# Kernel tuning notes

Hardware: AMD Instinct MI355X
Metric: run time of the kernel (lower is better)

## Reference

```python
import jax, jax.numpy as jnp
import numpy as np

HEADS = 8
LN_EPS = 1e-5


def _layernorm(x, g, b):
    mu = x.mean(-1, keepdims=True)
    var = jnp.var(x, axis=-1, keepdims=True)  # biased, matches torch LayerNorm
    return (x - mu) / jnp.sqrt(var + LN_EPS) * g + b


def setup_inputs() -> dict:
    key = jax.random.key(0)
    ks = jax.random.split(key, 5)
    Q, N, D = 4, 2048, 512  # [query-groups, tokens, model dim]
    return {
        "q": jax.random.normal(ks[0], (Q, N, D), jnp.float32),
        "k": jax.random.normal(ks[1], (Q, N, D), jnp.float32),
        "v": jax.random.normal(ks[2], (Q, N, D), jnp.float32),
        "ln_gamma": jnp.ones((D,), jnp.float32),
        "ln_beta": jnp.zeros((D,), jnp.float32),
        "w_in": jax.random.normal(ks[3], (D, D), jnp.float32) * 0.02,   # torch Linear weight [inner_dim, dim]
        "w_out": jax.random.normal(ks[4], (D, D), jnp.float32) * 0.02,  # [dim, inner_dim]
        "b_out": jnp.zeros((D,), jnp.float32),
        "cov_w_raw": jnp.float32(0.6),
        "var_w_raw": jnp.float32(0.2),
    }


def reference(q, k, v, ln_gamma, ln_beta, w_in, w_out, b_out, cov_w_raw, var_w_raw):
    H = HEADS

    def proj(t):
        x = _layernorm(t, ln_gamma, ln_beta) @ w_in.T  # [Q,N,inner]
        Qd, Nd, I = x.shape
        return x.reshape(Qd, Nd, H, I // H).transpose(2, 0, 1, 3)  # [H,Q,N,d]

    f_q, f_k, f_v = proj(q), proj(k), proj(v)
    d = f_q.shape[-1]

    # cosine similarity component
    dots = jnp.einsum('hqnd,hqmd->hqnm', f_q, f_k)
    qn = jnp.linalg.norm(f_q, axis=-1)  # [H,Q,N]
    kn = jnp.linalg.norm(f_k, axis=-1)
    cosine_sim = dots / (qn[..., :, None] * kn[..., None, :])

    # centered covariance component
    qc = f_q - f_q.mean(-1, keepdims=True)
    kc = f_k - f_k.mean(-1, keepdims=True)
    cov_component = jnp.einsum('hqnd,hqmd->hqnm', qc, kc) / d

    # variance product component (torch.var is unbiased -> ddof=1)
    q_var = jnp.var(f_q, axis=-1, ddof=1)  # [H,Q,N]
    k_var = jnp.var(f_k, axis=-1, ddof=1)
    var_component = q_var[..., :, None] * k_var[..., None, :] / d

    cov_w = jax.nn.sigmoid(cov_w_raw)
    var_w = jax.nn.sigmoid(var_w_raw)
    cos_w = 1.0 - cov_w - var_w
    attn = cos_w * cosine_sim + cov_w * cov_component + var_w * var_component

    out = jnp.einsum('hqnm,hqmd->hqnd', attn, f_v)
    out = out.transpose(1, 2, 0, 3).reshape(q.shape[0], q.shape[1], -1)  # q n (h d)
    return out @ w_out.T + b_out
```

## Files before the change

kernel.cpp:

```cpp
#include <hip/hip_runtime.h>
#include <hip/hip_bf16.h>
#include <math.h>

#define D_MODEL 512
#define NTOK 2048
#define QGRP 4
#define NHEAD 8
#define HDIM 64
#define ROWS_PER_T (QGRP * NTOK)
#define LN_EPS 1e-5f
#define NCHUNK 16

typedef __attribute__((ext_vector_type(8))) short short8;
typedef __attribute__((ext_vector_type(8))) __bf16 bf16x8;
typedef __attribute__((ext_vector_type(4))) float f32x4;

__device__ inline void split2(float y, ushort& h, ushort& l) {
    __hip_bfloat16 hb = __float2bfloat16(y);
    float hf = __bfloat162float(hb);
    __hip_bfloat16 lb = __float2bfloat16(y - hf);
    h = *reinterpret_cast<ushort*>(&hb);
    l = *reinterpret_cast<ushort*>(&lb);
}

__device__ inline float b2f(ushort u) {
    unsigned int x = ((unsigned int)u) << 16;
    return __uint_as_float(x);
}

__device__ inline void split8v(const float4& p0, const float4& p1, bf16x8& bh, bf16x8& bl) {
    float xv[8] = {p0.x, p0.y, p0.z, p0.w, p1.x, p1.y, p1.z, p1.w};
    ushort hs[8], ls[8];
#pragma unroll
    for (int j = 0; j < 8; ++j) split2(xv[j], hs[j], ls[j]);
    bh = *(const bf16x8*)hs;
    bl = *(const bf16x8*)ls;
}

__global__ __launch_bounds__(256)
void ln_split3_kernel(const float* __restrict__ q, const float* __restrict__ k,
                      const float* __restrict__ v, const float* __restrict__ gamma,
                      const float* __restrict__ beta,
                      ushort* __restrict__ A3h, ushort* __restrict__ A3l) {
    int wave = threadIdx.x >> 6, lane = threadIdx.x & 63;
    size_t row = (size_t)blockIdx.x * 4 + wave;
    int t = (int)(row >> 13);
    size_t r = row & 8191;
    const float* src = (t == 0 ? q : (t == 1 ? k : v)) + r * D_MODEL + lane * 8;
    float4 a = *(const float4*)src;
    float4 b = *(const float4*)(src + 4);
    float s  = a.x + a.y + a.z + a.w + b.x + b.y + b.z + b.w;
    float sq = a.x*a.x + a.y*a.y + a.z*a.z + a.w*a.w
             + b.x*b.x + b.y*b.y + b.z*b.z + b.w*b.w;
    for (int m = 1; m < 64; m <<= 1) {
        s  += __shfl_xor(s, m);
        sq += __shfl_xor(sq, m);
    }
    float mu   = s * (1.0f / (float)D_MODEL);
    float var  = sq * (1.0f / (float)D_MODEL) - mu * mu;
    float rstd = 1.0f / sqrtf(var + LN_EPS);
    float4 g0 = *(const float4*)(gamma + lane * 8);
    float4 g1 = *(const float4*)(gamma + lane * 8 + 4);
    float4 t0 = *(const float4*)(beta + lane * 8);
    float4 t1 = *(const float4*)(beta + lane * 8 + 4);
    float xv[8] = {a.x, a.y, a.z, a.w, b.x, b.y, b.z, b.w};
    float gv[8] = {g0.x, g0.y, g0.z, g0.w, g1.x, g1.y, g1.z, g1.w};
    float bv[8] = {t0.x, t0.y, t0.z, t0.w, t1.x, t1.y, t1.z, t1.w};
    ushort hs[8], ls[8];
#pragma unroll
    for (int j = 0; j < 8; ++j) {
        float y = (xv[j] - mu) * rstd * gv[j] + bv[j];
        split2(y, hs[j], ls[j]);
    }
    *(short8*)(A3h + row * D_MODEL + lane * 8) = *(const short8*)hs;
    *(short8*)(A3l + row * D_MODEL + lane * 8) = *(const short8*)ls;
}

__global__ __launch_bounds__(256)
void split_mat2_kernel(const float* __restrict__ W0, const float* __restrict__ W1,
                       ushort* __restrict__ Wh0, ushort* __restrict__ Wl0,
                       ushort* __restrict__ Wh1, ushort* __restrict__ Wl1) {
    int half = blockIdx.x >> 7;
    const float* W = half ? W1 : W0;
    ushort* Wh = half ? Wh1 : Wh0;
    ushort* Wl = half ? Wl1 : Wl0;
    size_t i = ((size_t)(blockIdx.x & 127) * 256 + threadIdx.x) * 8;
    float4 a = *(const float4*)(W + i);
    float4 b = *(const float4*)(W + i + 4);
    float xv[8] = {a.x, a.y, a.z, a.w, b.x, b.y, b.z, b.w};
    ushort hs[8], ls[8];
#pragma unroll
    for (int j = 0; j < 8; ++j) split2(xv[j], hs[j], ls[j]);
    *(short8*)(Wh + i) = *(const short8*)hs;
    *(short8*)(Wl + i) = *(const short8*)ls;
}

template <int MODE>
__global__ __launch_bounds__(256, 2)
void gemm_split_kernel(const ushort* __restrict__ Ah, const ushort* __restrict__ Al,
                       const ushort* __restrict__ Wh, const ushort* __restrict__ Wl,
                       const float* __restrict__ bias, float* __restrict__ C,
                       ushort* __restrict__ Ch, ushort* __restrict__ Cl) {
    __shared__ __align__(16) ushort sA[2][128][64];
    __shared__ __align__(16) ushort sW[2][128][64];
    int tid  = threadIdx.x;
    int lane = tid & 63, wid = tid >> 6;
    int wr = wid >> 1, wc = wid & 1;
    int z, xblk;
    if (MODE == 3) { z = blockIdx.x % 3; xblk = blockIdx.x / 3; }
    else           { z = 0;              xblk = blockIdx.x;     }
    size_t rowBase = (size_t)xblk * 128;
    size_t colBase = (size_t)blockIdx.y * 128;
    size_t zoff = (size_t)z * ROWS_PER_T * D_MODEL;
    const ushort* gA[2] = {Ah + zoff, Al + zoff};
    const ushort* gW[2] = {Wh, Wl};

    int sr = tid >> 3;
    int sc8 = tid & 7;

    short8 st[16];

#define LOADK(KT)                                                                  \
    {                                                                              \
        int idx = 0;                                                               \
        _Pragma("unroll")                                                          \
        for (int hl = 0; hl < 2; ++hl)                                             \
            _Pragma("unroll")                                                      \
            for (int p = 0; p < 4; ++p) {                                          \
                int r = p * 32 + sr;                                               \
                st[idx++] = *(const short8*)(gA[hl] + (rowBase + r) * D_MODEL +    \
                                             (KT) + sc8 * 8);                      \
            }                                                                      \
        _Pragma("unroll")                                                          \
        for (int hl = 0; hl < 2; ++hl)                                             \
            _Pragma("unroll")                                                      \
            for (int p = 0; p < 4; ++p) {                                          \
                int r = p * 32 + sr;                                               \
                st[idx++] = *(const short8*)(gW[hl] + (colBase + r) * D_MODEL +    \
                                             (KT) + sc8 * 8);                      \
            }                                                                      \
    }

    f32x4 acc[4][4] = {};

    LOADK(0);
    for (int step = 0; step < 8; ++step) {
        __syncthreads();
        {
            int idx = 0;
#pragma unroll
            for (int hl = 0; hl < 2; ++hl)
#pragma unroll
                for (int p = 0; p < 4; ++p) {
                    int r = p * 32 + sr;
                    *(short8*)&sA[hl][r][((sc8 ^ (r & 7)) << 3)] = st[idx++];
                }
#pragma unroll
            for (int hl = 0; hl < 2; ++hl)
#pragma unroll
                for (int p = 0; p < 4; ++p) {
                    int r = p * 32 + sr;
                    *(short8*)&sW[hl][r][((sc8 ^ (r & 7)) << 3)] = st[idx++];
                }
        }
        __syncthreads();
        if (step < 7) LOADK((step + 1) * 64);
#pragma unroll
        for (int sl = 0; sl < 2; ++sl) {
            bf16x8 aH[4], aL[4];
#pragma unroll
            for (int m = 0; m < 4; ++m) {
                int r = wr * 64 + m * 16 + (lane & 15);
                int cs = ((sl * 4 + (lane >> 4)) ^ (r & 7)) << 3;
                aH[m] = *(const bf16x8*)&sA[0][r][cs];
                aL[m] = *(const bf16x8*)&sA[1][r][cs];
            }
#pragma unroll
            for (int n = 0; n < 4; ++n) {
                int r = wc * 64 + n * 16 + (lane & 15);
                int cs = ((sl * 4 + (lane >> 4)) ^ (r & 7)) << 3;
                bf16x8 bH = *(const bf16x8*)&sW[0][r][cs];
                bf16x8 bL = *(const bf16x8*)&sW[1][r][cs];
#pragma unroll
                for (int m = 0; m < 4; ++m) {
                    acc[m][n] = __builtin_amdgcn_mfma_f32_16x16x32_bf16(aL[m], bH, acc[m][n], 0, 0, 0);
                    acc[m][n] = __builtin_amdgcn_mfma_f32_16x16x32_bf16(aH[m], bL, acc[m][n], 0, 0, 0);
                    acc[m][n] = __builtin_amdgcn_mfma_f32_16x16x32_bf16(aH[m], bH, acc[m][n], 0, 0, 0);
                }
            }
        }
    }
#pragma unroll
    for (int m = 0; m < 4; ++m)
#pragma unroll
        for (int n = 0; n < 4; ++n) {
            size_t col = colBase + wc * 64 + n * 16 + (lane & 15);
            size_t rb  = rowBase + wr * 64 + m * 16 + ((lane >> 4) << 2);
            if (MODE == 3) {
                if (z == 0) {
#pragma unroll
                    for (int r = 0; r < 4; ++r) {
                        ushort oh, ol;
                        split2(acc[m][n][r], oh, ol);
                        Ch[(rb + r) * D_MODEL + col] = oh;
                        Cl[(rb + r) * D_MODEL + col] = ol;
                    }
                } else {
                    float* Cz = C + (size_t)(z - 1) * ROWS_PER_T * D_MODEL;
#pragma unroll
                    for (int r = 0; r < 4; ++r)
                        Cz[(rb + r) * D_MODEL + col] = acc[m][n][r];
                }
            } else {
                float bv = bias[col];
#pragma unroll
                for (int r = 0; r < 4; ++r)
                    C[(rb + r) * D_MODEL + col] = acc[m][n][r] + bv;
            }
        }
#undef LOADK
}

__global__ __launch_bounds__(256)
void pair_reduce_mfma_kernel(const float* __restrict__ fk, const float* __restrict__ fv,
                             float* __restrict__ partials) {
    int pc = blockIdx.x;
    int pair = pc >> 4, chunk = pc & 15;
    int h = pair & 7, qg = pair >> 3;
    const float* Fk = fk + ((size_t)(qg * NTOK + chunk * 128)) * D_MODEL + h * HDIM;
    const float* Fv = fv + ((size_t)(qg * NTOK + chunk * 128)) * D_MODEL + h * HDIM;
    __shared__ float fkT[64][132];
    __shared__ float fvT[64][132];
    __shared__ float rkn_s[128], kvar_s[128];
    __shared__ float uvp[4][64];
    int tid = threadIdx.x, lane = tid & 63, wid = tid >> 6;
    int tn = tid >> 2;
    int fb = (tid & 3) << 2;
#pragma unroll
    for (int pass = 0; pass < 2; ++pass) {
        int n = pass * 64 + tn;
        float x[16], y[16];
#pragma unroll
        for (int j4 = 0; j4 < 4; ++j4) {
            *(float4*)&x[j4 * 4] = *(const float4*)(Fk + (size_t)n * D_MODEL + fb + j4 * 16);
            *(float4*)&y[j4 * 4] = *(const float4*)(Fv + (size_t)n * D_MODEL + fb + j4 * 16);
        }
        float s = 0.f, sq = 0.f;
#pragma unroll
        for (int j = 0; j < 16; ++j) { s += x[j]; sq += x[j] * x[j]; }
        s  += __shfl_xor(s, 1);  s  += __shfl_xor(s, 2);
        sq += __shfl_xor(sq, 1); sq += __shfl_xor(sq, 2);
        if ((tid & 3) == 0) {
            rkn_s[n]  = 1.0f / sqrtf(sq);
            kvar_s[n] = (sq - s * s * (1.0f / 64.0f)) * (1.0f / 63.0f);
        }
#pragma unroll
        for (int j4 = 0; j4 < 4; ++j4)
#pragma unroll
            for (int i = 0; i < 4; ++i) {
                fkT[fb + j4 * 16 + i][n] = x[j4 * 4 + i];
                fvT[fb + j4 * 16 + i][n] = y[j4 * 4 + i];
            }
    }
    __syncthreads();

    {
        float acc = 0.f;
#pragma unroll
        for (int j4 = 0; j4 < 8; ++j4) {
            float4 kv  = *(const float4*)&kvar_s[wid * 32 + j4 * 4];
            float4 f4  = *(const float4*)&fvT[lane][wid * 32 + j4 * 4];
            acc += kv.x * f4.x + kv.y * f4.y + kv.z * f4.z + kv.w * f4.w;
        }
        uvp[wid][lane] = acc;
    }

    int wm = wid >> 1, wn = wid & 1;
    int fr = lane & 15, kg = (lane >> 4) << 3;
    f32x4 accP[2][2] = {}, accC[2][2] = {};
#pragma unroll
    for (int t = 0; t < 4; ++t) {
        int k0 = t * 32 + kg;
        float4 rk0 = *(const float4*)&rkn_s[k0];
        float4 rk1 = *(const float4*)&rkn_s[k0 + 4];
        bf16x8 aRH[2], aRL[2], aSH[2], aSL[2], bH[2], bL[2];
#pragma unroll
        for (int m = 0; m < 2; ++m) {
            int a = wm * 32 + m * 16 + fr;
            float4 r0 = *(const float4*)&fkT[a][k0];
            float4 r1 = *(const float4*)&fkT[a][k0 + 4];
            split8v(r0, r1, aRH[m], aRL[m]);
            float4 s0 = make_float4(r0.x * rk0.x, r0.y * rk0.y, r0.z * rk0.z, r0.w * rk0.w);
            float4 s1 = make_float4(r1.x * rk1.x, r1.y * rk1.y, r1.z * rk1.z, r1.w * rk1.w);
            split8v(s0, s1, aSH[m], aSL[m]);
        }
#pragma unroll
        for (int n = 0; n < 2; ++n) {
            int c = wn * 32 + n * 16 + fr;
            float4 r0 = *(const float4*)&fvT[c][k0];
            float4 r1 = *(const float4*)&fvT[c][k0 + 4];
            split8v(r0, r1, bH[n], bL[n]);
        }
#pragma unroll
        for (int m = 0; m < 2; ++m)
#pragma unroll
            for (int n = 0; n < 2; ++n) {
                accP[m][n] = __builtin_amdgcn_mfma_f32_16x16x32_bf16(aSL[m], bH[n], accP[m][n], 0, 0, 0);
                accP[m][n] = __builtin_amdgcn_mfma_f32_16x16x32_bf16(aSH[m], bL[n], accP[m][n], 0, 0, 0);
                accP[m][n] = __builtin_amdgcn_mfma_f32_16x16x32_bf16(aSH[m], bH[n], accP[m][n], 0, 0, 0);
                accC[m][n] = __builtin_amdgcn_mfma_f32_16x16x32_bf16(aRL[m], bH[n], accC[m][n], 0, 0, 0);
                accC[m][n] = __builtin_amdgcn_mfma_f32_16x16x32_bf16(aRH[m], bL[n], accC[m][n], 0, 0, 0);
                accC[m][n] = __builtin_amdgcn_mfma_f32_16x16x32_bf16(aRH[m], bH[n], accC[m][n], 0, 0, 0);
            }
    }

    float* outp = partials + (size_t)pc * 8256;
#pragma unroll
    for (int m = 0; m < 2; ++m)
#pragma unroll
        for (int n = 0; n < 2; ++n) {
            int a0 = wm * 32 + m * 16 + ((lane >> 4) << 2);
            int c  = wn * 32 + n * 16 + fr;
#pragma unroll
            for (int r = 0; r < 4; ++r) {
                outp[(a0 + r) * 64 + c]        = accP[m][n][r];
                outp[4096 + (a0 + r) * 64 + c] = accC[m][n][r];
            }
        }
    __syncthreads();
    if (tid < 64)
        outp[8192 + tid] = uvp[0][tid] + uvp[1][tid] + uvp[2][tid] + uvp[3][tid];
}

__global__ __launch_bounds__(256)
void pair_finalize_kernel(const float* __restrict__ partials, float* __restrict__ pairacc) {
    int pair = blockIdx.x >> 3, sl = blockIdx.x & 7;
    int e0 = sl * 1032, e1 = e0 + 1032;
    for (int e = e0 + threadIdx.x; e < e1; e += 256) {
        float s = 0.f;
        for (int c = 0; c < NCHUNK; ++c)
            s += partials[((size_t)(pair * NCHUNK + c)) * 8256 + e];
        pairacc[(size_t)pair * 8320 + e] = s;
    }
}

__global__ __launch_bounds__(256)
void q_apply_mfma_kernel(const ushort* __restrict__ Fqh, const ushort* __restrict__ Fql,
                         const float* __restrict__ pairacc,
                         const float* __restrict__ cov_raw, const float* __restrict__ var_raw,
                         ushort* __restrict__ Oh, ushort* __restrict__ Ol) {
    int pair = blockIdx.x >> 4, chunk = blockIdx.x & 15;
    int h = pair & 7, qg = pair >> 3;
    __shared__ float PT[64][68];
    __shared__ float CT[64][68];
    __shared__ float u_s[64], sc_s[64];
    const float* pa = pairacc + (size_t)pair * 8320;
    for (int e = threadIdx.x; e < 4096; e += 256) {
        int a = e >> 6, c = e & 63;
        PT[c][a] = pa[e];
        CT[c][a] = pa[4096 + e];
    }
    if (threadIdx.x < 64) u_s[threadIdx.x] = pa[8192 + threadIdx.x];
    __syncthreads();
    if (threadIdx.x < 64) {
        float s = 0.f;
#pragma unroll
        for (int a = 0; a < 64; ++a) s += CT[threadIdx.x][a];
        sc_s[threadIdx.x] = s;
    }
    __syncthreads();
    int tid = threadIdx.x, lane = tid & 63, wave = tid >> 6;
    size_t row0 = (size_t)qg * NTOK + (size_t)chunk * 128 + wave * 32;
    const ushort* qhp = Fqh + row0 * D_MODEL + h * HDIM;
    const ushort* qlp = Fql + row0 * D_MODEL + h * HDIM;

    bf16x8 aH[2][2], aL[2][2];
    float qsum[2], qsq[2];
#pragma unroll
    for (int m = 0; m < 2; ++m) {
        int r = m * 16 + (lane & 15);
        int k0 = (lane >> 4) * 8;
        float s = 0.f, sq = 0.f;
#pragma unroll
        for (int ks = 0; ks < 2; ++ks) {
            short8 hv = *(const short8*)(qhp + (size_t)r * D_MODEL + ks * 32 + k0);
            short8 lv = *(const short8*)(qlp + (size_t)r * D_MODEL + ks * 32 + k0);
            aH[m][ks] = *(const bf16x8*)&hv;
            aL[m][ks] = *(const bf16x8*)&lv;
#pragma unroll
            for (int j = 0; j < 8; ++j) {
                float val = b2f((ushort)hv[j]) + b2f((ushort)lv[j]);
                s += val; sq += val * val;
            }
        }
        s  += __shfl_xor(s, 16);  s  += __shfl_xor(s, 32);
        sq += __shfl_xor(sq, 16); sq += __shfl_xor(sq, 32);
        qsum[m] = s; qsq[m] = sq;
    }

    f32x4 accP[2][4] = {}, accC[2][4] = {};
#pragma unroll
    for (int n = 0; n < 4; ++n) {
        int c = n * 16 + (lane & 15);
#pragma unroll
        for (int ks = 0; ks < 2; ++ks) {
            int kb = ks * 32 + (lane >> 4) * 8;
            {
                float4 p0 = *(const float4*)&PT[c][kb];
                float4 p1 = *(const float4*)&PT[c][kb + 4];
                bf16x8 bH, bL;
                split8v(p0, p1, bH, bL);
#pragma unroll
                for (int m = 0; m < 2; ++m) {
                    accP[m][n] = __builtin_amdgcn_mfma_f32_16x16x32_bf16(aL[m][ks], bH, accP[m][n], 0, 0, 0);
                    accP[m][n] = __builtin_amdgcn_mfma_f32_16x16x32_bf16(aH[m][ks], bL, accP[m][n], 0, 0, 0);
                    accP[m][n] = __builtin_amdgcn_mfma_f32_16x16x32_bf16(aH[m][ks], bH, accP[m][n], 0, 0, 0);
                }
            }
            {
                float4 p0 = *(const float4*)&CT[c][kb];
                float4 p1 = *(const float4*)&CT[c][kb + 4];
                bf16x8 bH, bL;
                split8v(p0, p1, bH, bL);
#pragma unroll
                for (int m = 0; m < 2; ++m) {
                    accC[m][n] = __builtin_amdgcn_mfma_f32_16x16x32_bf16(aL[m][ks], bH, accC[m][n], 0, 0, 0);
                    accC[m][n] = __builtin_amdgcn_mfma_f32_16x16x32_bf16(aH[m][ks], bL, accC[m][n], 0, 0, 0);
                    accC[m][n] = __builtin_amdgcn_mfma_f32_16x16x32_bf16(aH[m][ks], bH, accC[m][n], 0, 0, 0);
                }
            }
        }
    }

    float cw = 1.0f / (1.0f + expf(-cov_raw[0]));
    float vw = 1.0f / (1.0f + expf(-var_raw[0]));
    float cos_w = 1.0f - cw - vw;
    float cw_cov = cw * (1.0f / 64.0f);
    float cw_var = vw * (1.0f / 64.0f);
#pragma unroll
    for (int n = 0; n < 4; ++n) {
        int c = n * 16 + (lane & 15);
        float u_c  = u_s[c];
        float sc_c = sc_s[c];
#pragma unroll
        for (int m = 0; m < 2; ++m)
#pragma unroll
            for (int i = 0; i < 4; ++i) {
                int rp = ((lane >> 4) << 2) + i;
                float s  = __shfl(qsum[m], rp);
                float sq = __shfl(qsq[m], rp);
                float qmean = s * (1.0f / 64.0f);
                float rqn   = 1.0f / sqrtf(sq);
                float qvar  = (sq - s * qmean) * (1.0f / 63.0f);
                float res = cos_w * rqn * accP[m][n][i]
                          + cw_cov * (accC[m][n][i] - qmean * sc_c)
                          + cw_var * qvar * u_c;
                ushort oh, ol;
                split2(res, oh, ol);
                size_t o = (row0 + m * 16 + rp) * D_MODEL + h * HDIM + c;
                Oh[o] = oh;
                Ol[o] = ol;
            }
    }
}

extern "C" void kernel_launch(void* const* d_in, const int* in_sizes, int n_in,
                              void* d_out, int out_size, void* d_ws, size_t ws_size,
                              hipStream_t stream) {
    const float* q     = (const float*)d_in[0];
    const float* k     = (const float*)d_in[1];
    const float* v     = (const float*)d_in[2];
    const float* gamma = (const float*)d_in[3];
    const float* beta  = (const float*)d_in[4];
    const float* w_in  = (const float*)d_in[5];
    const float* w_out = (const float*)d_in[6];
    const float* b_out = (const float*)d_in[7];
    const float* cov_r = (const float*)d_in[8];
    const float* var_r = (const float*)d_in[9];
    float* out = (float*)d_out;

    const size_t E = (size_t)ROWS_PER_T * D_MODEL;
    float*  ws       = (float*)d_ws;
    float*  fk       = ws;
    float*  fv       = fk + E;
    ushort* Fqh      = (ushort*)(fv + E);
    ushort* Fql      = Fqh + E;
    ushort* A3h      = Fql + E;
    ushort* A3l      = A3h + 3 * E;
    ushort* Whi      = A3l + 3 * E;
    ushort* Wli      = Whi + D_MODEL * D_MODEL;
    ushort* Who      = Wli + D_MODEL * D_MODEL;
    ushort* Wlo      = Who + D_MODEL * D_MODEL;
    ushort* Oh       = Wlo + D_MODEL * D_MODEL;
    ushort* Ol       = Oh + E;
    float*  partials = (float*)(Ol + E);
    float*  pairacc  = partials + (size_t)32 * NCHUNK * 8256;

    hipLaunchKernelGGL(split_mat2_kernel, dim3(256), dim3(256), 0, stream,
                       w_in, w_out, Whi, Wli, Who, Wlo);
    hipLaunchKernelGGL(ln_split3_kernel, dim3(3 * ROWS_PER_T / 4), dim3(256), 0, stream,
                       q, k, v, gamma, beta, A3h, A3l);
    hipLaunchKernelGGL((gemm_split_kernel<3>), dim3(192, 4), dim3(256), 0, stream,
                       A3h, A3l, Whi, Wli, (const float*)nullptr, fk, Fqh, Fql);
    hipLaunchKernelGGL(pair_reduce_mfma_kernel, dim3(32 * NCHUNK), dim3(256), 0, stream,
                       fk, fv, partials);
    hipLaunchKernelGGL(pair_finalize_kernel, dim3(32 * 8), dim3(256), 0, stream,
                       partials, pairacc);
    hipLaunchKernelGGL(q_apply_mfma_kernel, dim3(512), dim3(256), 0, stream,
                       Fqh, Fql, pairacc, cov_r, var_r, Oh, Ol);
    hipLaunchKernelGGL((gemm_split_kernel<2>), dim3(ROWS_PER_T / 128, 4), dim3(256), 0, stream,
                       Oh, Ol, Who, Wlo, b_out, out, (ushort*)nullptr, (ushort*)nullptr);
}
```

Measured before the change: 117.0 us.

## Fuse LayerNorm and bf16 split into input projection GEMM prologue

The separate LayerNorm+split kernel is removed. The projection GEMM now reads fp32 q/k/v directly, computes per-row mean and rstd in a prologue, and normalizes and splits into hi/lo bf16 while staging tiles into shared memory. This drops the write and re-read of the 3x bf16 hi/lo activation buffers. The GEMM also moves to 512 threads with 8 waves of 64x32 tiles instead of 4 waves of 64x64, which lowers per-thread register pressure. In exchange, each block re-reads its rows for the statistics pass, the normalization is recomputed once per column block (4x), and the old occupancy hint of 2 blocks per CU is dropped.

```diff
diff --git a/kernel.cpp b/kernel.cpp
--- a/kernel.cpp
+++ b/kernel.cpp
@@ -35,45 +35,6 @@
     for (int j = 0; j < 8; ++j) split2(xv[j], hs[j], ls[j]);
     bh = *(const bf16x8*)hs;
     bl = *(const bf16x8*)ls;
-}
-
-__global__ __launch_bounds__(256)
-void ln_split3_kernel(const float* __restrict__ q, const float* __restrict__ k,
-                      const float* __restrict__ v, const float* __restrict__ gamma,
-                      const float* __restrict__ beta,
-                      ushort* __restrict__ A3h, ushort* __restrict__ A3l) {
-    int wave = threadIdx.x >> 6, lane = threadIdx.x & 63;
-    size_t row = (size_t)blockIdx.x * 4 + wave;
-    int t = (int)(row >> 13);
-    size_t r = row & 8191;
-    const float* src = (t == 0 ? q : (t == 1 ? k : v)) + r * D_MODEL + lane * 8;
-    float4 a = *(const float4*)src;
-    float4 b = *(const float4*)(src + 4);
-    float s  = a.x + a.y + a.z + a.w + b.x + b.y + b.z + b.w;
-    float sq = a.x*a.x + a.y*a.y + a.z*a.z + a.w*a.w
-             + b.x*b.x + b.y*b.y + b.z*b.z + b.w*b.w;
-    for (int m = 1; m < 64; m <<= 1) {
-        s  += __shfl_xor(s, m);
-        sq += __shfl_xor(sq, m);
-    }
-    float mu   = s * (1.0f / (float)D_MODEL);
-    float var  = sq * (1.0f / (float)D_MODEL) - mu * mu;
-    float rstd = 1.0f / sqrtf(var + LN_EPS);
-    float4 g0 = *(const float4*)(gamma + lane * 8);
-    float4 g1 = *(const float4*)(gamma + lane * 8 + 4);
-    float4 t0 = *(const float4*)(beta + lane * 8);
-    float4 t1 = *(const float4*)(beta + lane * 8 + 4);
-    float xv[8] = {a.x, a.y, a.z, a.w, b.x, b.y, b.z, b.w};
-    float gv[8] = {g0.x, g0.y, g0.z, g0.w, g1.x, g1.y, g1.z, g1.w};
-    float bv[8] = {t0.x, t0.y, t0.z, t0.w, t1.x, t1.y, t1.z, t1.w};
-    ushort hs[8], ls[8];
-#pragma unroll
-    for (int j = 0; j < 8; ++j) {
-        float y = (xv[j] - mu) * rstd * gv[j] + bv[j];
-        split2(y, hs[j], ls[j]);
-    }
-    *(short8*)(A3h + row * D_MODEL + lane * 8) = *(const short8*)hs;
-    *(short8*)(A3l + row * D_MODEL + lane * 8) = *(const short8*)ls;
 }
 
 __global__ __launch_bounds__(256)
@@ -96,75 +57,138 @@
 }
 
 template <int MODE>
-__global__ __launch_bounds__(256, 2)
-void gemm_split_kernel(const ushort* __restrict__ Ah, const ushort* __restrict__ Al,
+__global__ __launch_bounds__(512)
+void gemm_split_kernel(const float* __restrict__ Qp, const float* __restrict__ Kp,
+                       const float* __restrict__ Vp,
+                       const float* __restrict__ gamma, const float* __restrict__ beta,
+                       const ushort* __restrict__ Ahx, const ushort* __restrict__ Alx,
                        const ushort* __restrict__ Wh, const ushort* __restrict__ Wl,
                        const float* __restrict__ bias, float* __restrict__ C,
                        ushort* __restrict__ Ch, ushort* __restrict__ Cl) {
     __shared__ __align__(16) ushort sA[2][128][64];
     __shared__ __align__(16) ushort sW[2][128][64];
+    __shared__ float sG[512], sB[512];
+    __shared__ float mu_s[128], rs_s[128];
+
     int tid  = threadIdx.x;
     int lane = tid & 63, wid = tid >> 6;
-    int wr = wid >> 1, wc = wid & 1;
+    int wr = wid >> 2, wc = wid & 3;
     int z, xblk;
     if (MODE == 3) { z = blockIdx.x % 3; xblk = blockIdx.x / 3; }
     else           { z = 0;              xblk = blockIdx.x;     }
     size_t rowBase = (size_t)xblk * 128;
     size_t colBase = (size_t)blockIdx.y * 128;
-    size_t zoff = (size_t)z * ROWS_PER_T * D_MODEL;
-    const ushort* gA[2] = {Ah + zoff, Al + zoff};
+
+    const float* srcA = nullptr;
+    const ushort* gAh = nullptr; const ushort* gAl = nullptr;
+    if (MODE == 3) {
+        srcA = (z == 0 ? Qp : (z == 1 ? Kp : Vp)) + rowBase * D_MODEL;
+    } else {
+        gAh = Ahx + rowBase * D_MODEL;
+        gAl = Alx + rowBase * D_MODEL;
+    }
     const ushort* gW[2] = {Wh, Wl};
 
-    int sr = tid >> 3;
-    int sc8 = tid & 7;
-
-    short8 st[16];
-
-#define LOADK(KT)                                                                  \
-    {                                                                              \
-        int idx = 0;                                                               \
-        _Pragma("unroll")                                                          \
-        for (int hl = 0; hl < 2; ++hl)                                             \
-            _Pragma("unroll")                                                      \
-            for (int p = 0; p < 4; ++p) {                                          \
-                int r = p * 32 + sr;                                               \
-                st[idx++] = *(const short8*)(gA[hl] + (rowBase + r) * D_MODEL +    \
-                                             (KT) + sc8 * 8);                      \
-            }                                                                      \
-        _Pragma("unroll")                                                          \
-        for (int hl = 0; hl < 2; ++hl)                                             \
-            _Pragma("unroll")                                                      \
-            for (int p = 0; p < 4; ++p) {                                          \
-                int r = p * 32 + sr;                                               \
-                st[idx++] = *(const short8*)(gW[hl] + (colBase + r) * D_MODEL +    \
-                                             (KT) + sc8 * 8);                      \
-            }                                                                      \
-    }
-
-    f32x4 acc[4][4] = {};
+    int sr = tid >> 3, sc8 = tid & 7;
+
+    float4 stA[2][2];
+    short8 stA16[2][2];
+    short8 stW[2][2];
+
+#define LOADK(KT)                                                                    \
+    {                                                                                \
+        if (MODE == 3) {                                                             \
+            _Pragma("unroll")                                                        \
+            for (int p = 0; p < 2; ++p) {                                            \
+                int r = p * 64 + sr;                                                 \
+                const float* ap = srcA + (size_t)r * D_MODEL + (KT) + sc8 * 8;       \
+                stA[p][0] = *(const float4*)ap;                                      \
+                stA[p][1] = *(const float4*)(ap + 4);                                \
+            }                                                                        \
+        } else {                                                                     \
+            _Pragma("unroll")                                                        \
+            for (int hl = 0; hl < 2; ++hl)                                           \
+                _Pragma("unroll")                                                    \
+                for (int p = 0; p < 2; ++p) {                                        \
+                    int r = p * 64 + sr;                                             \
+                    stA16[hl][p] = *(const short8*)((hl ? gAl : gAh) +               \
+                                    (size_t)r * D_MODEL + (KT) + sc8 * 8);           \
+                }                                                                    \
+        }                                                                            \
+        _Pragma("unroll")                                                            \
+        for (int hl = 0; hl < 2; ++hl)                                               \
+            _Pragma("unroll")                                                        \
+            for (int p = 0; p < 2; ++p) {                                            \
+                int r = p * 64 + sr;                                                 \
+                stW[hl][p] = *(const short8*)(gW[hl] + (colBase + r) * D_MODEL +     \
+                                              (KT) + sc8 * 8);                       \
+            }                                                                        \
+    }
 
     LOADK(0);
+
+    if (MODE == 3) {
+        sG[tid] = gamma[tid];
+        sB[tid] = beta[tid];
+        int r = tid >> 2, qd = tid & 3;
+        const float* rp = srcA + (size_t)r * D_MODEL + qd * 128;
+        float s = 0.f, sq = 0.f;
+#pragma unroll
+        for (int j = 0; j < 32; ++j) {
+            float4 a4 = *(const float4*)(rp + j * 4);
+            s  += a4.x + a4.y + a4.z + a4.w;
+            sq += a4.x*a4.x + a4.y*a4.y + a4.z*a4.z + a4.w*a4.w;
+        }
+        s  += __shfl_xor(s, 1);  s  += __shfl_xor(s, 2);
+        sq += __shfl_xor(sq, 1); sq += __shfl_xor(sq, 2);
+        if (qd == 0) {
+            float mu = s * (1.0f / (float)D_MODEL);
+            mu_s[r] = mu;
+            rs_s[r] = rsqrtf(sq * (1.0f / (float)D_MODEL) - mu * mu + LN_EPS);
+        }
+    }
+
+    f32x4 acc[4][2] = {};
+
     for (int step = 0; step < 8; ++step) {
+        int KT = step * 64;
         __syncthreads();
-        {
-            int idx = 0;
+        if (MODE == 3) {
+#pragma unroll
+            for (int p = 0; p < 2; ++p) {
+                int r = p * 64 + sr;
+                float mu = mu_s[r], rs = rs_s[r];
+                float xv[8];
+                *(float4*)&xv[0] = stA[p][0];
+                *(float4*)&xv[4] = stA[p][1];
+                ushort hs[8], ls[8];
+#pragma unroll
+                for (int j = 0; j < 8; ++j) {
+                    int cc = KT + sc8 * 8 + j;
+                    float yv = (xv[j] - mu) * rs * sG[cc] + sB[cc];
+                    split2(yv, hs[j], ls[j]);
+                }
+                *(short8*)&sA[0][r][(sc8 ^ (r & 7)) << 3] = *(const short8*)hs;
+                *(short8*)&sA[1][r][(sc8 ^ (r & 7)) << 3] = *(const short8*)ls;
+            }
+        } else {
 #pragma unroll
             for (int hl = 0; hl < 2; ++hl)
 #pragma unroll
-                for (int p = 0; p < 4; ++p) {
-                    int r = p * 32 + sr;
-                    *(short8*)&sA[hl][r][((sc8 ^ (r & 7)) << 3)] = st[idx++];
+                for (int p = 0; p < 2; ++p) {
+                    int r = p * 64 + sr;
+                    *(short8*)&sA[hl][r][(sc8 ^ (r & 7)) << 3] = stA16[hl][p];
                 }
-#pragma unroll
-            for (int hl = 0; hl < 2; ++hl)
-#pragma unroll
-                for (int p = 0; p < 4; ++p) {
-                    int r = p * 32 + sr;
-                    *(short8*)&sW[hl][r][((sc8 ^ (r & 7)) << 3)] = st[idx++];
-                }
-        }
+        }
+#pragma unroll
+        for (int hl = 0; hl < 2; ++hl)
+#pragma unroll
+            for (int p = 0; p < 2; ++p) {
+                int r = p * 64 + sr;
+                *(short8*)&sW[hl][r][(sc8 ^ (r & 7)) << 3] = stW[hl][p];
+            }
         __syncthreads();
-        if (step < 7) LOADK((step + 1) * 64);
+        if (step < 7) LOADK(KT + 64);
 #pragma unroll
         for (int sl = 0; sl < 2; ++sl) {
             bf16x8 aH[4], aL[4];
@@ -176,11 +200,11 @@
                 aL[m] = *(const bf16x8*)&sA[1][r][cs];
             }
 #pragma unroll
-            for (int n = 0; n < 4; ++n) {
-                int r = wc * 64 + n * 16 + (lane & 15);
-                int cs = ((sl * 4 + (lane >> 4)) ^ (r & 7)) << 3;
-                bf16x8 bH = *(const bf16x8*)&sW[0][r][cs];
-                bf16x8 bL = *(const bf16x8*)&sW[1][r][cs];
+            for (int n = 0; n < 2; ++n) {
+                int rc = wc * 32 + n * 16 + (lane & 15);
+                int cs = ((sl * 4 + (lane >> 4)) ^ (rc & 7)) << 3;
+                bf16x8 bH = *(const bf16x8*)&sW[0][rc][cs];
+                bf16x8 bL = *(const bf16x8*)&sW[1][rc][cs];
 #pragma unroll
                 for (int m = 0; m < 4; ++m) {
                     acc[m][n] = __builtin_amdgcn_mfma_f32_16x16x32_bf16(aL[m], bH, acc[m][n], 0, 0, 0);
@@ -193,8 +217,8 @@
 #pragma unroll
     for (int m = 0; m < 4; ++m)
 #pragma unroll
-        for (int n = 0; n < 4; ++n) {
-            size_t col = colBase + wc * 64 + n * 16 + (lane & 15);
+        for (int n = 0; n < 2; ++n) {
+            size_t col = colBase + wc * 32 + n * 16 + (lane & 15);
             size_t rb  = rowBase + wr * 64 + m * 16 + ((lane >> 4) << 2);
             if (MODE == 3) {
                 if (z == 0) {
@@ -485,9 +509,7 @@
     float*  fv       = fk + E;
     ushort* Fqh      = (ushort*)(fv + E);
     ushort* Fql      = Fqh + E;
-    ushort* A3h      = Fql + E;
-    ushort* A3l      = A3h + 3 * E;
-    ushort* Whi      = A3l + 3 * E;
+    ushort* Whi      = Fql + E;
     ushort* Wli      = Whi + D_MODEL * D_MODEL;
     ushort* Who      = Wli + D_MODEL * D_MODEL;
     ushort* Wlo      = Who + D_MODEL * D_MODEL;
@@ -498,16 +520,17 @@
 
     hipLaunchKernelGGL(split_mat2_kernel, dim3(256), dim3(256), 0, stream,
                        w_in, w_out, Whi, Wli, Who, Wlo);
-    hipLaunchKernelGGL(ln_split3_kernel, dim3(3 * ROWS_PER_T / 4), dim3(256), 0, stream,
-                       q, k, v, gamma, beta, A3h, A3l);
-    hipLaunchKernelGGL((gemm_split_kernel<3>), dim3(192, 4), dim3(256), 0, stream,
-                       A3h, A3l, Whi, Wli, (const float*)nullptr, fk, Fqh, Fql);
+    hipLaunchKernelGGL((gemm_split_kernel<3>), dim3(192, 4), dim3(512), 0, stream,
+                       q, k, v, gamma, beta, (const ushort*)nullptr, (const ushort*)nullptr,
+                       Whi, Wli, (const float*)nullptr, fk, Fqh, Fql);
     hipLaunchKernelGGL(pair_reduce_mfma_kernel, dim3(32 * NCHUNK), dim3(256), 0, stream,
                        fk, fv, partials);
     hipLaunchKernelGGL(pair_finalize_kernel, dim3(32 * 8), dim3(256), 0, stream,
                        partials, pairacc);
     hipLaunchKernelGGL(q_apply_mfma_kernel, dim3(512), dim3(256), 0, stream,
                        Fqh, Fql, pairacc, cov_r, var_r, Oh, Ol);
-    hipLaunchKernelGGL((gemm_split_kernel<2>), dim3(ROWS_PER_T / 128, 4), dim3(256), 0, stream,
-                       Oh, Ol, Who, Wlo, b_out, out, (ushort*)nullptr, (ushort*)nullptr);
-}
+    hipLaunchKernelGGL((gemm_split_kernel<2>), dim3(ROWS_PER_T / 128, 4), dim3(512), 0, stream,
+                       (const float*)nullptr, (const float*)nullptr, (const float*)nullptr,
+                       (const float*)nullptr, (const float*)nullptr, Oh, Ol,
+                       Who, Wlo, b_out, out, (ushort*)nullptr, (ushort*)nullptr);
+}
```

After: 121.7 us. 4.0% more time.
